# Kernel tuning notes

Hardware: AMD Instinct MI355X
Metric: run time of the kernel (lower is better)

Reference implementation:

```python
import jax, jax.numpy as jnp
import numpy as np

# Model dims (match init_kwargs)
D_MODEL = 512
NUM_EXPERTS = 8
TOP_K = 2
FFN_MULT = 2
HIDDEN = FFN_MULT * D_MODEL
BATCH, SEQ = 4, 2048


def setup_inputs() -> dict:
    key = jax.random.key(0)
    k_x, k_g, k_bg, k_w1, k_w3, k_w2 = jax.random.split(key, 6)
    sd = 1.0 / np.sqrt(D_MODEL).astype(np.float32)
    sh = 1.0 / np.sqrt(HIDDEN).astype(np.float32)
    return {
        "x": jax.random.normal(k_x, (BATCH, SEQ, D_MODEL), dtype=jnp.float32),
        # gate: nn.Linear(d_model, num_experts) with bias
        "Wg": jax.random.normal(k_g, (D_MODEL, NUM_EXPERTS), dtype=jnp.float32) * sd,
        "bg": jax.random.normal(k_bg, (NUM_EXPERTS,), dtype=jnp.float32) * 0.01,
        # stacked per-expert SwiGLU FFN params (no bias, LLaMA-style)
        "W1": jax.random.normal(k_w1, (NUM_EXPERTS, D_MODEL, HIDDEN), dtype=jnp.float32) * sd,
        "W3": jax.random.normal(k_w3, (NUM_EXPERTS, D_MODEL, HIDDEN), dtype=jnp.float32) * sd,
        "W2": jax.random.normal(k_w2, (NUM_EXPERTS, HIDDEN, D_MODEL), dtype=jnp.float32) * sh,
    }


def reference(x, Wg, bg, W1, W3, W2):
    B, S, D = x.shape
    E = Wg.shape[1]
    xt = x.reshape(-1, D)                        # [T, D], T = B*S
    T = xt.shape[0]

    # Router: top-k over experts, softmax over the k selected logits
    logits = xt @ Wg + bg                        # [T, E]
    top_vals, top_idx = jax.lax.top_k(logits, TOP_K)  # [T, K]
    top_probs = jax.nn.softmax(top_vals, axis=-1)     # [T, K]

    # Dense per-(token, expert) combine weight; zero where expert not selected.
    # top-k indices are distinct per token so scatter-add == scatter-set.
    gate_w = jnp.zeros((T, E), dtype=xt.dtype).at[
        jnp.arange(T)[:, None], top_idx
    ].add(top_probs)                              # [T, E]

    # Loop over experts (fixed, small), accumulate weighted expert outputs.
    def body(y, expert):
        w1, w3, w2, g = expert                   # g: [T]
        h = jax.nn.silu(xt @ w1) * (xt @ w3)     # [T, H]
        return y + g[:, None] * (h @ w2), None

    y0 = jnp.zeros_like(xt)
    y, _ = jax.lax.scan(body, y0, (W1, W3, W2, gate_w.T))
    return y.reshape(B, S, D)
```

## Files before the change

### kernel.cpp

```cpp
#include <hip/hip_runtime.h>
#include <hip/hip_bf16.h>

#define TOKENS 8192
#define DM 512
#define NE 8
#define HID 1024
#define NSLOT (TOKENS * 2)
#define NB 32

#define BM 128
#define BN 64
#define BK 64
#define MAXTILE 136

typedef __bf16 bf16x8 __attribute__((ext_vector_type(8)));
typedef float floatx4 __attribute__((ext_vector_type(4)));
typedef unsigned short u16x8 __attribute__((ext_vector_type(8)));

__device__ __forceinline__ unsigned short f2bf(float f) {
    union { float f; unsigned u; } c; c.f = f;
    unsigned u = c.u;
    u += 0x7fffu + ((u >> 16) & 1u);
    return (unsigned short)(u >> 16);
}

__device__ __forceinline__ void load16_lds(const void* g, void* l) {
    __builtin_amdgcn_global_load_lds(
        (const __attribute__((address_space(1))) unsigned int*)g,
        (__attribute__((address_space(3))) unsigned int*)l, 16, 0, 0);
}

__global__ void cvt_transpose_kernel(const float* __restrict__ W1, const float* __restrict__ W3,
                                     const float* __restrict__ W2,
                                     unsigned short* __restrict__ w1t, unsigned short* __restrict__ w3t,
                                     unsigned short* __restrict__ w2t) {
    __shared__ float tile[64][65];
    const float* src; unsigned short* dst; int K, N;
    if (blockIdx.y == 0)      { src = W1; dst = w1t; K = DM;  N = HID; }
    else if (blockIdx.y == 1) { src = W3; dst = w3t; K = DM;  N = HID; }
    else                      { src = W2; dst = w2t; K = HID; N = DM;  }
    const int tkn = (K >> 6) * (N >> 6);
    int b = blockIdx.x;
    int e = b / tkn;
    int rem = b % tkn;
    const int tn6 = N >> 6;
    int kt = rem / tn6, nt = rem % tn6;
    int tx = threadIdx.x & 15, ty = threadIdx.x >> 4;
    const float* s = src + ((size_t)(e * K + kt * 64 + ty)) * N + nt * 64 + tx * 4;
    #pragma unroll
    for (int i = 0; i < 4; i++) {
        float4 v = *(const float4*)(s + (size_t)(i * 16) * N);
        float* tr = &tile[ty + i * 16][tx * 4];
        tr[0] = v.x; tr[1] = v.y; tr[2] = v.z; tr[3] = v.w;
    }
    __syncthreads();
    int n = threadIdx.x >> 3;
    int c8 = (threadIdx.x & 7) * 8;
    unsigned short* d = dst + ((size_t)(e * N + nt * 64)) * K + kt * 64;
    #pragma unroll
    for (int i = 0; i < 2; i++) {
        int nn = n + i * 32;
        u16x8 r;
        #pragma unroll
        for (int kk = 0; kk < 8; kk++) r[kk] = f2bf(tile[c8 + kk][nn]);
        *(u16x8*)(d + (size_t)nn * K + c8) = r;
    }
}

__global__ void router_kernel(const float* __restrict__ x, const float* __restrict__ Wg,
                              const float* __restrict__ bg,
                              int* __restrict__ top_idx, float* __restrict__ top_p,
                              unsigned short* __restrict__ xb) {
    int lane = threadIdx.x & 63, wave = threadIdx.x >> 6;
    int t = blockIdx.x * 4 + wave;
    const float4* xr4 = (const float4*)(x + (size_t)t * DM) + lane * 2;
    float4 va = xr4[0], vb = xr4[1];
    float xv[8] = {va.x, va.y, va.z, va.w, vb.x, vb.y, vb.z, vb.w};
    u16x8 r;
    #pragma unroll
    for (int j = 0; j < 8; j++) r[j] = f2bf(xv[j]);
    *((u16x8*)(xb + (size_t)t * DM) + lane) = r;

    float acc[NE];
    #pragma unroll
    for (int e = 0; e < NE; e++) acc[e] = 0.f;
    #pragma unroll
    for (int j = 0; j < 8; j++) {
        int d = lane * 8 + j;
        const float4* wr = (const float4*)(Wg + (size_t)d * NE);
        float4 w0 = wr[0], w1 = wr[1];
        float xvj = xv[j];
        acc[0] += xvj * w0.x; acc[1] += xvj * w0.y; acc[2] += xvj * w0.z; acc[3] += xvj * w0.w;
        acc[4] += xvj * w1.x; acc[5] += xvj * w1.y; acc[6] += xvj * w1.z; acc[7] += xvj * w1.w;
    }
    #pragma unroll
    for (int e = 0; e < NE; e++) {
        float v = acc[e];
        #pragma unroll
        for (int off = 32; off > 0; off >>= 1) v += __shfl_down(v, off, 64);
        acc[e] = v;
    }
    if (lane == 0) {
        float best = -1e30f, second = -1e30f;
        int bi = 0, si = 0;
        #pragma unroll
        for (int e = 0; e < NE; e++) {
            float v = acc[e] + bg[e];
            if (v > best) { second = best; si = bi; best = v; bi = e; }
            else if (v > second) { second = v; si = e; }
        }
        float ex = __expf(second - best);
        float inv = 1.f / (1.f + ex);
        top_idx[t * 2] = bi;  top_idx[t * 2 + 1] = si;
        top_p[t * 2] = inv;   top_p[t * 2 + 1] = ex * inv;
    }
}

__global__ void hist_kernel(const int* __restrict__ top_idx, int* __restrict__ block_hist) {
    __shared__ int h[NE];
    int b = blockIdx.x, tid = threadIdx.x;
    if (tid < NE) h[tid] = 0;
    __syncthreads();
    int t = b * 256 + tid;
    atomicAdd(&h[top_idx[t * 2]], 1);
    atomicAdd(&h[top_idx[t * 2 + 1]], 1);
    __syncthreads();
    if (tid < NE) block_hist[b * NE + tid] = h[tid];
}

__global__ void build_kernel(const int* __restrict__ top_idx, const float* __restrict__ top_p,
                             const int* __restrict__ block_hist,
                             int* __restrict__ rows, float* __restrict__ gates,
                             int* __restrict__ slot_of,
                             int* __restrict__ counts, int* __restrict__ offsets) {
    __shared__ int hist_s[NB * NE];
    __shared__ int tot_s[NE];
    __shared__ int offs_s[NE];
    __shared__ int cur[NE];
    int b = blockIdx.x, tid = threadIdx.x;
    if (tid < NB * NE) hist_s[tid] = block_hist[tid];
    __syncthreads();
    int mybase = 0;
    if (tid < NE) {
        int run = 0;
        for (int bb = 0; bb < NB; bb++) {
            if (bb == b) mybase = run;
            run += hist_s[bb * NE + tid];
        }
        tot_s[tid] = run;
    }
    __syncthreads();
    if (tid == 0) {
        int s = 0;
        for (int e = 0; e < NE; e++) { offs_s[e] = s; s += tot_s[e]; }
    }
    __syncthreads();
    if (tid < NE) {
        cur[tid] = offs_s[tid] + mybase;
        if (b == 0) { counts[tid] = tot_s[tid]; offsets[tid] = offs_s[tid]; }
    }
    __syncthreads();
    int t = b * 256 + tid;
    #pragma unroll
    for (int k = 0; k < 2; k++) {
        int e = top_idx[t * 2 + k];
        int slot = atomicAdd(&cur[e], 1);
        rows[slot] = t;
        gates[slot] = top_p[t * 2 + k];
        slot_of[t * 2 + k] = slot;
    }
}

__device__ __forceinline__ bool tile_lookup(const int* counts, const int* offsets, int gy,
                                            int& e, int& mt, int& cnt, int& off) {
    int bacc = 0;
    #pragma unroll
    for (int ee = 0; ee < NE; ee++) {
        int c = counts[ee];
        int ntl = (c + BM - 1) >> 7;
        if (gy < bacc + ntl) { e = ee; mt = gy - bacc; cnt = c; off = offsets[ee]; return true; }
        bacc += ntl;
    }
    return false;
}

__global__ __launch_bounds__(256) void gemm1_kernel(
    const unsigned short* __restrict__ xb,
    const unsigned short* __restrict__ w1t,
    const unsigned short* __restrict__ w3t,
    unsigned short* __restrict__ Hb,
    const int* __restrict__ rows, const int* __restrict__ counts,
    const int* __restrict__ offsets) {
    const int lid = blockIdx.x;
    const int xcd = lid & 7;
    const int j = lid >> 3;
    const int gy = xcd * (MAXTILE / 8) + (j >> 4);
    const int nt = j & 15;
    int e, mt, cnt, off;
    if (!tile_lookup(counts, offsets, gy, e, mt, cnt, off)) return;

    __shared__ unsigned short As[2][BM * BK];
    __shared__ unsigned short B1s[2][BN * BK];
    __shared__ unsigned short B3s[2][BN * BK];

    const int tid = threadIdx.x;
    const int lane = tid & 63, wave = tid >> 6;
    const int lrow8 = lane >> 3;
    const int lchunk = (lane & 7) ^ lrow8;

    const unsigned short* a_g[4];
    #pragma unroll
    for (int i = 0; i < 4; i++) {
        int r = (wave * 4 + i) * 8 + lrow8;
        int gr = mt * BM + r;
        int tok = rows[off + (gr < cnt ? gr : 0)];
        a_g[i] = xb + (size_t)tok * DM + lchunk * 8;
    }
    const unsigned short* b1_g[2]; const unsigned short* b3_g[2];
    #pragma unroll
    for (int i = 0; i < 2; i++) {
        int r = (wave * 2 + i) * 8 + lrow8;
        b1_g[i] = w1t + ((size_t)e * HID + nt * BN + r) * DM + lchunk * 8;
        b3_g[i] = w3t + ((size_t)e * HID + nt * BN + r) * DM + lchunk * 8;
    }

    const int l15 = lane & 15, quad = lane >> 4;
    const int sw = l15 & 7;

    floatx4 acc1[2][4], acc3[2][4];
    #pragma unroll
    for (int i = 0; i < 2; i++)
        #pragma unroll
        for (int j2 = 0; j2 < 4; j2++) {
            acc1[i][j2] = (floatx4){0.f, 0.f, 0.f, 0.f};
            acc3[i][j2] = (floatx4){0.f, 0.f, 0.f, 0.f};
        }

    auto stage = [&](int k0, int b) {
        #pragma unroll
        for (int i = 0; i < 4; i++) load16_lds(a_g[i] + k0, &As[b][(wave * 4 + i) * 512]);
        #pragma unroll
        for (int i = 0; i < 2; i++) {
            load16_lds(b1_g[i] + k0, &B1s[b][(wave * 2 + i) * 512]);
            load16_lds(b3_g[i] + k0, &B3s[b][(wave * 2 + i) * 512]);
        }
    };
    auto compute = [&](int b) {
        #pragma unroll
        for (int kk = 0; kk < 2; kk++) {
            const int qc = kk * 4 + quad;
            const int ch = (qc ^ sw) << 3;
            bf16x8 af[2], b1f[4], b3f[4];
            #pragma unroll
            for (int mi = 0; mi < 2; mi++)
                af[mi] = *(const bf16x8*)(&As[b][(wave * 32 + mi * 16 + l15) * 64 + ch]);
            #pragma unroll
            for (int ni = 0; ni < 4; ni++) {
                b1f[ni] = *(const bf16x8*)(&B1s[b][(ni * 16 + l15) * 64 + ch]);
                b3f[ni] = *(const bf16x8*)(&B3s[b][(ni * 16 + l15) * 64 + ch]);
            }
            #pragma unroll
            for (int mi = 0; mi < 2; mi++)
                #pragma unroll
                for (int ni = 0; ni < 4; ni++) {
                    acc1[mi][ni] = __builtin_amdgcn_mfma_f32_16x16x32_bf16(af[mi], b1f[ni], acc1[mi][ni], 0, 0, 0);
                    acc3[mi][ni] = __builtin_amdgcn_mfma_f32_16x16x32_bf16(af[mi], b3f[ni], acc3[mi][ni], 0, 0, 0);
                }
        }
    };

    const int NI = DM / BK;
    stage(0, 0);
    #pragma unroll
    for (int i = 0; i < NI; i += 2) {
        __syncthreads();
        if (i + 1 < NI) stage((i + 1) * BK, 1);
        compute(0);
        __syncthreads();
        if (i + 2 < NI) stage((i + 2) * BK, 0);
        compute(1);
    }
    #pragma unroll
    for (int mi = 0; mi < 2; mi++) {
        #pragma unroll
        for (int r = 0; r < 4; r++) {
            int mloc = wave * 32 + mi * 16 + quad * 4 + r;
            int gi = mt * BM + mloc;
            if (gi < cnt) {
                size_t rowbase = (size_t)(off + gi) * HID + nt * BN;
                #pragma unroll
                for (int ni = 0; ni < 4; ni++) {
                    float z1 = acc1[mi][ni][r];
                    float z3 = acc3[mi][ni][r];
                    float h = (z1 / (1.f + __expf(-z1))) * z3;
                    Hb[rowbase + ni * 16 + l15] = f2bf(h);
                }
            }
        }
    }
}

__global__ __launch_bounds__(256) void gemm2_kernel(
    const unsigned short* __restrict__ Hb,
    const unsigned short* __restrict__ w2t,
    unsigned short* __restrict__ P,
    const float* __restrict__ gates,
    const int* __restrict__ counts, const int* __restrict__ offsets) {
    const int lid = blockIdx.x;
    const int xcd = lid & 7;
    const int j = lid >> 3;
    const int gy = xcd * (MAXTILE / 8) + (j >> 3);
    const int nt = j & 7;
    int e, mt, cnt, off;
    if (!tile_lookup(counts, offsets, gy, e, mt, cnt, off)) return;

    __shared__ unsigned short As[2][BM * BK];
    __shared__ unsigned short Bs[2][BN * BK];

    const int tid = threadIdx.x;
    const int lane = tid & 63, wave = tid >> 6;
    const int lrow8 = lane >> 3;
    const int lchunk = (lane & 7) ^ lrow8;

    const unsigned short* a_g[4];
    #pragma unroll
    for (int i = 0; i < 4; i++) {
        int r = (wave * 4 + i) * 8 + lrow8;
        int sl = off + mt * BM + r;
        if (sl >= NSLOT) sl = NSLOT - 1;
        a_g[i] = Hb + (size_t)sl * HID + lchunk * 8;
    }
    const unsigned short* b_g[2];
    #pragma unroll
    for (int i = 0; i < 2; i++) {
        int r = (wave * 2 + i) * 8 + lrow8;
        b_g[i] = w2t + ((size_t)e * DM + nt * BN + r) * HID + lchunk * 8;
    }

    const int l15 = lane & 15, quad = lane >> 4;
    const int sw = l15 & 7;

    floatx4 acc[2][4];
    #pragma unroll
    for (int i = 0; i < 2; i++)
        #pragma unroll
        for (int j2 = 0; j2 < 4; j2++) acc[i][j2] = (floatx4){0.f, 0.f, 0.f, 0.f};

    auto stage = [&](int k0, int b) {
        #pragma unroll
        for (int i = 0; i < 4; i++) load16_lds(a_g[i] + k0, &As[b][(wave * 4 + i) * 512]);
        #pragma unroll
        for (int i = 0; i < 2; i++) load16_lds(b_g[i] + k0, &Bs[b][(wave * 2 + i) * 512]);
    };
    auto compute = [&](int b) {
        #pragma unroll
        for (int kk = 0; kk < 2; kk++) {
            const int qc = kk * 4 + quad;
            const int ch = (qc ^ sw) << 3;
            bf16x8 af[2], bf[4];
            #pragma unroll
            for (int mi = 0; mi < 2; mi++)
                af[mi] = *(const bf16x8*)(&As[b][(wave * 32 + mi * 16 + l15) * 64 + ch]);
            #pragma unroll
            for (int ni = 0; ni < 4; ni++)
                bf[ni] = *(const bf16x8*)(&Bs[b][(ni * 16 + l15) * 64 + ch]);
            #pragma unroll
            for (int mi = 0; mi < 2; mi++)
                #pragma unroll
                for (int ni = 0; ni < 4; ni++)
                    acc[mi][ni] = __builtin_amdgcn_mfma_f32_16x16x32_bf16(af[mi], bf[ni], acc[mi][ni], 0, 0, 0);
        }
    };

    const int NI = HID / BK;
    stage(0, 0);
    #pragma unroll
    for (int i = 0; i < NI; i += 2) {
        __syncthreads();
        if (i + 1 < NI) stage((i + 1) * BK, 1);
        compute(0);
        __syncthreads();
        if (i + 2 < NI) stage((i + 2) * BK, 0);
        compute(1);
    }
    #pragma unroll
    for (int mi = 0; mi < 2; mi++) {
        #pragma unroll
        for (int r = 0; r < 4; r++) {
            int mloc = wave * 32 + mi * 16 + quad * 4 + r;
            int gi = mt * BM + mloc;
            if (gi < cnt) {
                int slot = off + gi;
                float g = gates[slot];
                #pragma unroll
                for (int ni = 0; ni < 4; ni++) {
                    int col = nt * BN + ni * 16 + l15;
                    P[(size_t)slot * DM + col] = f2bf(g * acc[mi][ni][r]);
                }
            }
        }
    }
}

__global__ void combine_kernel(const unsigned short* __restrict__ P,
                               const int* __restrict__ slot_of, float* __restrict__ y) {
    int i = blockIdx.x * blockDim.x + threadIdx.x;
    int t = i / (DM / 8);
    int c8 = i % (DM / 8);
    int s0 = slot_of[t * 2], s1 = slot_of[t * 2 + 1];
    uint4 a = *(const uint4*)(P + (size_t)s0 * DM + c8 * 8);
    uint4 b = *(const uint4*)(P + (size_t)s1 * DM + c8 * 8);
    float o[8];
    const unsigned* aw = (const unsigned*)&a;
    const unsigned* bw = (const unsigned*)&b;
    #pragma unroll
    for (int j = 0; j < 4; j++) {
        union { unsigned u; float f; } al, ah, bl, bh;
        al.u = aw[j] << 16; ah.u = aw[j] & 0xffff0000u;
        bl.u = bw[j] << 16; bh.u = bw[j] & 0xffff0000u;
        o[j * 2]     = al.f + bl.f;
        o[j * 2 + 1] = ah.f + bh.f;
    }
    float4* yo = (float4*)(y + (size_t)t * DM + c8 * 8);
    yo[0] = make_float4(o[0], o[1], o[2], o[3]);
    yo[1] = make_float4(o[4], o[5], o[6], o[7]);
}

extern "C" void kernel_launch(void* const* d_in, const int* in_sizes, int n_in,
                              void* d_out, int out_size, void* d_ws, size_t ws_size,
                              hipStream_t stream) {
    (void)in_sizes; (void)n_in; (void)out_size; (void)ws_size;
    const float* x  = (const float*)d_in[0];
    const float* Wg = (const float*)d_in[1];
    const float* bg = (const float*)d_in[2];
    const float* W1 = (const float*)d_in[3];
    const float* W3 = (const float*)d_in[4];
    const float* W2 = (const float*)d_in[5];
    float* y = (float*)d_out;

    char* p = (char*)d_ws;
    auto carve = [&](size_t bytes) -> char* {
        char* r = p;
        p += (bytes + 255) & ~(size_t)255;
        return r;
    };
    unsigned short* xb   = (unsigned short*)carve((size_t)TOKENS * DM * 2);
    unsigned short* w1t  = (unsigned short*)carve((size_t)NE * DM * HID * 2);
    unsigned short* w3t  = (unsigned short*)carve((size_t)NE * DM * HID * 2);
    unsigned short* w2t  = (unsigned short*)carve((size_t)NE * HID * DM * 2);
    unsigned short* Hb   = (unsigned short*)carve((size_t)NSLOT * HID * 2);
    int*   rows    = (int*)carve(NSLOT * 4);
    float* gates   = (float*)carve(NSLOT * 4);
    int*   slot_of = (int*)carve(NSLOT * 4);
    int*   tidx    = (int*)carve((size_t)TOKENS * 2 * 4);
    float* tp      = (float*)carve((size_t)TOKENS * 2 * 4);
    int*   counts  = (int*)carve(256);
    int*   offsets = (int*)carve(256);
    int*   bhist   = (int*)carve((size_t)NB * NE * 4);
    unsigned short* P = w1t;

    router_kernel<<<dim3(TOKENS / 4), dim3(256), 0, stream>>>(x, Wg, bg, tidx, tp, xb);
    cvt_transpose_kernel<<<dim3(NE * 8 * 16, 3), dim3(256), 0, stream>>>(W1, W3, W2, w1t, w3t, w2t);
    hist_kernel<<<dim3(NB), dim3(256), 0, stream>>>(tidx, bhist);
    build_kernel<<<dim3(NB), dim3(256), 0, stream>>>(tidx, tp, bhist, rows, gates, slot_of, counts, offsets);
    gemm1_kernel<<<dim3((HID / BN) * MAXTILE), dim3(256), 0, stream>>>(xb, w1t, w3t, Hb, rows, counts, offsets);
    gemm2_kernel<<<dim3((DM / BN) * MAXTILE), dim3(256), 0, stream>>>(Hb, w2t, P, gates, counts, offsets);
    combine_kernel<<<dim3((TOKENS * DM / 8) / 256), dim3(256), 0, stream>>>(P, slot_of, y);
}
```

Measured before the change: 225.1 us.

## Replace LDS-staged GEMM tiles with direct global-to-register operand loads

Both grouped GEMM kernels drop the shared-memory double buffers and the global_load_lds staging. Instead, each lane loads its MFMA fragments straight from global memory with a one-step register prefetch. This removes the barriers and the LDS round trip. In exchange, operand reuse across waves through LDS is lost, global loads become narrower and strided, and latency hiding depends on a single prefetch stage.

```diff
diff --git a/kernel.cpp b/kernel.cpp
--- a/kernel.cpp
+++ b/kernel.cpp
@@ -10,7 +10,6 @@
 
 #define BM 128
 #define BN 64
-#define BK 64
 #define MAXTILE 136
 
 typedef __bf16 bf16x8 __attribute__((ext_vector_type(8)));
@@ -22,12 +21,6 @@
     unsigned u = c.u;
     u += 0x7fffu + ((u >> 16) & 1u);
     return (unsigned short)(u >> 16);
-}
-
-__device__ __forceinline__ void load16_lds(const void* g, void* l) {
-    __builtin_amdgcn_global_load_lds(
-        (const __attribute__((address_space(1))) unsigned int*)g,
-        (__attribute__((address_space(3))) unsigned int*)l, 16, 0, 0);
 }
 
 __global__ void cvt_transpose_kernel(const float* __restrict__ W1, const float* __restrict__ W3,
@@ -199,33 +192,24 @@
     int e, mt, cnt, off;
     if (!tile_lookup(counts, offsets, gy, e, mt, cnt, off)) return;
 
-    __shared__ unsigned short As[2][BM * BK];
-    __shared__ unsigned short B1s[2][BN * BK];
-    __shared__ unsigned short B3s[2][BN * BK];
-
-    const int tid = threadIdx.x;
-    const int lane = tid & 63, wave = tid >> 6;
-    const int lrow8 = lane >> 3;
-    const int lchunk = (lane & 7) ^ lrow8;
-
-    const unsigned short* a_g[4];
-    #pragma unroll
-    for (int i = 0; i < 4; i++) {
-        int r = (wave * 4 + i) * 8 + lrow8;
-        int gr = mt * BM + r;
+    const int lane = threadIdx.x & 63, wave = threadIdx.x >> 6;
+    const int l15 = lane & 15, quad = lane >> 4;
+
+    const unsigned short* aP[2];
+    #pragma unroll
+    for (int mi = 0; mi < 2; mi++) {
+        int gr = mt * BM + wave * 32 + mi * 16 + l15;
         int tok = rows[off + (gr < cnt ? gr : 0)];
-        a_g[i] = xb + (size_t)tok * DM + lchunk * 8;
-    }
-    const unsigned short* b1_g[2]; const unsigned short* b3_g[2];
-    #pragma unroll
-    for (int i = 0; i < 2; i++) {
-        int r = (wave * 2 + i) * 8 + lrow8;
-        b1_g[i] = w1t + ((size_t)e * HID + nt * BN + r) * DM + lchunk * 8;
-        b3_g[i] = w3t + ((size_t)e * HID + nt * BN + r) * DM + lchunk * 8;
-    }
-
-    const int l15 = lane & 15, quad = lane >> 4;
-    const int sw = l15 & 7;
+        aP[mi] = xb + (size_t)tok * DM + quad * 8;
+    }
+    const unsigned short* b1P[4];
+    const unsigned short* b3P[4];
+    #pragma unroll
+    for (int ni = 0; ni < 4; ni++) {
+        size_t rb = ((size_t)e * HID + nt * BN + ni * 16 + l15) * DM + quad * 8;
+        b1P[ni] = w1t + rb;
+        b3P[ni] = w3t + rb;
+    }
 
     floatx4 acc1[2][4], acc3[2][4];
     #pragma unroll
@@ -236,50 +220,41 @@
             acc3[i][j2] = (floatx4){0.f, 0.f, 0.f, 0.f};
         }
 
-    auto stage = [&](int k0, int b) {
-        #pragma unroll
-        for (int i = 0; i < 4; i++) load16_lds(a_g[i] + k0, &As[b][(wave * 4 + i) * 512]);
-        #pragma unroll
-        for (int i = 0; i < 2; i++) {
-            load16_lds(b1_g[i] + k0, &B1s[b][(wave * 2 + i) * 512]);
-            load16_lds(b3_g[i] + k0, &B3s[b][(wave * 2 + i) * 512]);
-        }
-    };
-    auto compute = [&](int b) {
-        #pragma unroll
-        for (int kk = 0; kk < 2; kk++) {
-            const int qc = kk * 4 + quad;
-            const int ch = (qc ^ sw) << 3;
-            bf16x8 af[2], b1f[4], b3f[4];
-            #pragma unroll
-            for (int mi = 0; mi < 2; mi++)
-                af[mi] = *(const bf16x8*)(&As[b][(wave * 32 + mi * 16 + l15) * 64 + ch]);
+    bf16x8 aC[2], b1C[4], b3C[4], aN[2], b1N[4], b3N[4];
+    #pragma unroll
+    for (int mi = 0; mi < 2; mi++) aC[mi] = *(const bf16x8*)(aP[mi]);
+    #pragma unroll
+    for (int ni = 0; ni < 4; ni++) {
+        b1C[ni] = *(const bf16x8*)(b1P[ni]);
+        b3C[ni] = *(const bf16x8*)(b3P[ni]);
+    }
+
+    const int NPH = DM / 32;
+    #pragma unroll
+    for (int ph = 0; ph < NPH; ph++) {
+        if (ph + 1 < NPH) {
+            int ko = (ph + 1) * 32;
+            #pragma unroll
+            for (int mi = 0; mi < 2; mi++) aN[mi] = *(const bf16x8*)(aP[mi] + ko);
             #pragma unroll
             for (int ni = 0; ni < 4; ni++) {
-                b1f[ni] = *(const bf16x8*)(&B1s[b][(ni * 16 + l15) * 64 + ch]);
-                b3f[ni] = *(const bf16x8*)(&B3s[b][(ni * 16 + l15) * 64 + ch]);
+                b1N[ni] = *(const bf16x8*)(b1P[ni] + ko);
+                b3N[ni] = *(const bf16x8*)(b3P[ni] + ko);
             }
-            #pragma unroll
-            for (int mi = 0; mi < 2; mi++)
-                #pragma unroll
-                for (int ni = 0; ni < 4; ni++) {
-                    acc1[mi][ni] = __builtin_amdgcn_mfma_f32_16x16x32_bf16(af[mi], b1f[ni], acc1[mi][ni], 0, 0, 0);
-                    acc3[mi][ni] = __builtin_amdgcn_mfma_f32_16x16x32_bf16(af[mi], b3f[ni], acc3[mi][ni], 0, 0, 0);
-                }
-        }
-    };
-
-    const int NI = DM / BK;
-    stage(0, 0);
-    #pragma unroll
-    for (int i = 0; i < NI; i += 2) {
-        __syncthreads();
-        if (i + 1 < NI) stage((i + 1) * BK, 1);
-        compute(0);
-        __syncthreads();
-        if (i + 2 < NI) stage((i + 2) * BK, 0);
-        compute(1);
-    }
+        }
+        #pragma unroll
+        for (int mi = 0; mi < 2; mi++)
+            #pragma unroll
+            for (int ni = 0; ni < 4; ni++) {
+                acc1[mi][ni] = __builtin_amdgcn_mfma_f32_16x16x32_bf16(aC[mi], b1C[ni], acc1[mi][ni], 0, 0, 0);
+                acc3[mi][ni] = __builtin_amdgcn_mfma_f32_16x16x32_bf16(aC[mi], b3C[ni], acc3[mi][ni], 0, 0, 0);
+            }
+        #pragma unroll
+        for (int mi = 0; mi < 2; mi++) aC[mi] = aN[mi];
+        #pragma unroll
+        for (int ni = 0; ni < 4; ni++) { b1C[ni] = b1N[ni]; b3C[ni] = b3N[ni]; }
+    }
+
     #pragma unroll
     for (int mi = 0; mi < 2; mi++) {
         #pragma unroll
@@ -314,31 +289,20 @@
     int e, mt, cnt, off;
     if (!tile_lookup(counts, offsets, gy, e, mt, cnt, off)) return;
 
-    __shared__ unsigned short As[2][BM * BK];
-    __shared__ unsigned short Bs[2][BN * BK];
-
-    const int tid = threadIdx.x;
-    const int lane = tid & 63, wave = tid >> 6;
-    const int lrow8 = lane >> 3;
-    const int lchunk = (lane & 7) ^ lrow8;
-
-    const unsigned short* a_g[4];
-    #pragma unroll
-    for (int i = 0; i < 4; i++) {
-        int r = (wave * 4 + i) * 8 + lrow8;
-        int sl = off + mt * BM + r;
+    const int lane = threadIdx.x & 63, wave = threadIdx.x >> 6;
+    const int l15 = lane & 15, quad = lane >> 4;
+
+    const unsigned short* aP[2];
+    #pragma unroll
+    for (int mi = 0; mi < 2; mi++) {
+        int sl = off + mt * BM + wave * 32 + mi * 16 + l15;
         if (sl >= NSLOT) sl = NSLOT - 1;
-        a_g[i] = Hb + (size_t)sl * HID + lchunk * 8;
-    }
-    const unsigned short* b_g[2];
-    #pragma unroll
-    for (int i = 0; i < 2; i++) {
-        int r = (wave * 2 + i) * 8 + lrow8;
-        b_g[i] = w2t + ((size_t)e * DM + nt * BN + r) * HID + lchunk * 8;
-    }
-
-    const int l15 = lane & 15, quad = lane >> 4;
-    const int sw = l15 & 7;
+        aP[mi] = Hb + (size_t)sl * HID + quad * 8;
+    }
+    const unsigned short* bP[4];
+    #pragma unroll
+    for (int ni = 0; ni < 4; ni++)
+        bP[ni] = w2t + ((size_t)e * DM + nt * BN + ni * 16 + l15) * HID + quad * 8;
 
     floatx4 acc[2][4];
     #pragma unroll
@@ -346,43 +310,33 @@
         #pragma unroll
         for (int j2 = 0; j2 < 4; j2++) acc[i][j2] = (floatx4){0.f, 0.f, 0.f, 0.f};
 
-    auto stage = [&](int k0, int b) {
-        #pragma unroll
-        for (int i = 0; i < 4; i++) load16_lds(a_g[i] + k0, &As[b][(wave * 4 + i) * 512]);
-        #pragma unroll
-        for (int i = 0; i < 2; i++) load16_lds(b_g[i] + k0, &Bs[b][(wave * 2 + i) * 512]);
-    };
-    auto compute = [&](int b) {
-        #pragma unroll
-        for (int kk = 0; kk < 2; kk++) {
-            const int qc = kk * 4 + quad;
-            const int ch = (qc ^ sw) << 3;
-            bf16x8 af[2], bf[4];
-            #pragma unroll
-            for (int mi = 0; mi < 2; mi++)
-                af[mi] = *(const bf16x8*)(&As[b][(wave * 32 + mi * 16 + l15) * 64 + ch]);
+    bf16x8 aC[2], bC[4], aN[2], bN[4];
+    #pragma unroll
+    for (int mi = 0; mi < 2; mi++) aC[mi] = *(const bf16x8*)(aP[mi]);
+    #pragma unroll
+    for (int ni = 0; ni < 4; ni++) bC[ni] = *(const bf16x8*)(bP[ni]);
+
+    const int NPH = HID / 32;
+    #pragma unroll 8
+    for (int ph = 0; ph < NPH; ph++) {
+        if (ph + 1 < NPH) {
+            int ko = (ph + 1) * 32;
+            #pragma unroll
+            for (int mi = 0; mi < 2; mi++) aN[mi] = *(const bf16x8*)(aP[mi] + ko);
+            #pragma unroll
+            for (int ni = 0; ni < 4; ni++) bN[ni] = *(const bf16x8*)(bP[ni] + ko);
+        }
+        #pragma unroll
+        for (int mi = 0; mi < 2; mi++)
             #pragma unroll
             for (int ni = 0; ni < 4; ni++)
-                bf[ni] = *(const bf16x8*)(&Bs[b][(ni * 16 + l15) * 64 + ch]);
-            #pragma unroll
-            for (int mi = 0; mi < 2; mi++)
-                #pragma unroll
-                for (int ni = 0; ni < 4; ni++)
-                    acc[mi][ni] = __builtin_amdgcn_mfma_f32_16x16x32_bf16(af[mi], bf[ni], acc[mi][ni], 0, 0, 0);
-        }
-    };
-
-    const int NI = HID / BK;
-    stage(0, 0);
-    #pragma unroll
-    for (int i = 0; i < NI; i += 2) {
-        __syncthreads();
-        if (i + 1 < NI) stage((i + 1) * BK, 1);
-        compute(0);
-        __syncthreads();
-        if (i + 2 < NI) stage((i + 2) * BK, 0);
-        compute(1);
-    }
+                acc[mi][ni] = __builtin_amdgcn_mfma_f32_16x16x32_bf16(aC[mi], bC[ni], acc[mi][ni], 0, 0, 0);
+        #pragma unroll
+        for (int mi = 0; mi < 2; mi++) aC[mi] = aN[mi];
+        #pragma unroll
+        for (int ni = 0; ni < 4; ni++) bC[ni] = bN[ni];
+    }
+
     #pragma unroll
     for (int mi = 0; mi < 2; mi++) {
         #pragma unroll
```

After: 409.7 us. +82.0%, slower.
